# Kernel optimization log

Hardware: AMD Instinct MI355X
Metric: run time of the kernel (lower is better)

Reference implementation:

```python
import jax, jax.numpy as jnp
import numpy as np

N_NODES = 100000
N_EDGES = 1600000
D_FEAT = 128
HIDDEN = 64
N_CLASSES = 40
NEG_SLOPE = 0.01  # jax.nn.leaky_relu default, matches flax nn.leaky_relu


def glorot(key, shape):
    fan_in, fan_out = shape
    return jax.random.normal(key, shape, dtype=jnp.float32) * jnp.sqrt(2.0 / (fan_in + fan_out))


def setup_inputs() -> dict:
    key = jax.random.key(0)
    ks = jax.random.split(key, 8)
    nodes = jax.random.normal(ks[0], (N_NODES, D_FEAT), dtype=jnp.float32)
    senders = jax.random.randint(ks[1], (N_EDGES,), 0, N_NODES, dtype=jnp.int32)
    receivers = jax.random.randint(ks[2], (N_EDGES,), 0, N_NODES, dtype=jnp.int32)
    W1 = glorot(ks[3], (D_FEAT, HIDDEN))
    b1 = jnp.zeros((HIDDEN,), jnp.float32)
    W2 = glorot(ks[4], (HIDDEN, HIDDEN))
    b2 = jnp.zeros((HIDDEN,), jnp.float32)
    W3 = glorot(ks[5], (HIDDEN, N_CLASSES))
    b3 = jnp.zeros((N_CLASSES,), jnp.float32)
    return {"nodes": nodes, "senders": senders, "receivers": receivers,
            "W1": W1, "b1": b1, "W2": W2, "b2": b2, "W3": W3, "b3": b3}


def gcn_aggregate(x, senders, receivers, n_nodes):
    """jraph.GraphConvolution symmetric_normalization aggregation (post update_node_fn)."""
    ones = jnp.ones(senders.shape[0], dtype=x.dtype)
    sender_deg = jax.ops.segment_sum(ones, senders, num_segments=n_nodes)
    receiver_deg = jax.ops.segment_sum(ones, receivers, num_segments=n_nodes)
    x = x * jax.lax.rsqrt(jnp.maximum(sender_deg, 1.0))[:, None]
    x = jax.ops.segment_sum(x[senders], receivers, num_segments=n_nodes)  # [N, F]
    x = x * jax.lax.rsqrt(jnp.maximum(receiver_deg, 1.0))[:, None]
    return x


def reference(nodes, senders, receivers, W1, b1, W2, b2, W3, b3):
    n = nodes.shape[0]
    # Layer 1: GraphConvolution(MLP([hidden, hidden], leaky_relu))
    h = jax.nn.leaky_relu(nodes @ W1 + b1, NEG_SLOPE)
    h = jax.nn.leaky_relu(h @ W2 + b2, NEG_SLOPE)
    h = gcn_aggregate(h, senders, receivers, n)
    # Dropout is deterministic (training=False) -> identity
    # Layer 2: GraphConvolution(Dense(number_classes))
    h = h @ W3 + b3
    h = gcn_aggregate(h, senders, receivers, n)
    return jax.nn.softmax(h, axis=-1)
```

## Files before the change

### kernel.cpp

```cpp
#include <hip/hip_runtime.h>
#include <hip/hip_fp16.h>

#define NEG_SLOPE 0.01f
#define RANGE_BITS 15
#define RANGE (1 << RANGE_BITS)
#define HWORDS (RANGE / 2)
#define SLICE_BITS 16
#define SLICE (1 << SLICE_BITS)

typedef _Float16 f16x8 __attribute__((ext_vector_type(8)));
typedef float f32x4 __attribute__((ext_vector_type(4)));

__device__ __forceinline__ float lrelu(float x) { return x > 0.f ? x : NEG_SLOPE * x; }

__device__ __forceinline__ unsigned pack2h(float a, float b) {
    __half2 h = __floats2half2_rn(a, b);
    unsigned u; __builtin_memcpy(&u, &h, 4); return u;
}
__device__ __forceinline__ float2 unpack2(unsigned u) {
    __half2 h = *reinterpret_cast<__half2*>(&u);
    return __half22float2(h);
}
__device__ __forceinline__ f16x8 u4h8(uint4 u) {
    f16x8 r; __builtin_memcpy(&r, &u, 16); return r;
}

__global__ __launch_bounds__(1024) void count_kernel(
    const int* __restrict__ snd, const int* __restrict__ rcv,
    unsigned* __restrict__ partial, unsigned short* __restrict__ pos16,
    int nE, int NR, int NS)
{
    __shared__ unsigned hist[HWORDS];
    const int b = blockIdx.x;
    const int a = b / (NR * NS);
    const int rem = b - a * NR * NS;
    const int r = rem / NS;
    const int s = rem - r * NS;
    const int t = threadIdx.x;
    for (int k = t; k < HWORDS; k += 1024) hist[k] = 0u;
    __syncthreads();
    const int base = r << RANGE_BITS;
    const int lo = s << SLICE_BITS;
    const int hi = min(lo + SLICE, nE);
    if (a == 0) {
        for (int i = lo + t; i < hi; i += 1024) {
            const int v = rcv[i];
            const unsigned d = (unsigned)(v - base);
            if (d < (unsigned)RANGE) {
                const unsigned sh = (d & 1u) << 4;
                const unsigned old = atomicAdd(&hist[d >> 1], 1u << sh);
                pos16[i] = (unsigned short)((old >> sh) & 0xffffu);
            }
        }
    } else {
        for (int i = lo + t; i < hi; i += 1024) {
            const int v = snd[i];
            const unsigned d = (unsigned)(v - base);
            if (d < (unsigned)RANGE) atomicAdd(&hist[d >> 1], 1u << ((d & 1u) << 4));
        }
    }
    __syncthreads();
    unsigned* dst = partial + (size_t)((a * NR + r) * NS + s) * HWORDS;
    for (int k = t; k < HWORDS; k += 1024) dst[k] = hist[k];
}

__global__ __launch_bounds__(256) void scanp_kernel(
    unsigned* __restrict__ partial,
    int* __restrict__ dr_i,
    float* __restrict__ rin, float* __restrict__ rout,
    int nN, int NR, int NS)
{
    const int gid = blockIdx.x * 256 + threadIdx.x;
    if (gid >= NR * HWORDS) return;
    const int r  = gid >> (RANGE_BITS - 1);
    const int wd = gid & (HWORDS - 1);
    unsigned* prcv = partial + (size_t)(r * NS) * HWORDS + wd;
    unsigned run0 = 0, run1 = 0;
    for (int s = 0; s < NS; ++s) {
        unsigned* p = prcv + (size_t)s * HWORDS;
        const unsigned c = *p;
        *p = run0 | (run1 << 16);
        run0 += c & 0xffffu;
        run1 += c >> 16;
    }
    const unsigned* psnd = partial + (size_t)((NR + r) * NS) * HWORDS + wd;
    unsigned t0 = 0, t1 = 0;
    for (int s = 0; s < NS; ++s) {
        const unsigned c = psnd[(size_t)s * HWORDS];
        t0 += c & 0xffffu;
        t1 += c >> 16;
    }
    const int n0 = (r << RANGE_BITS) + 2 * wd;
    if (n0 < nN) {
        dr_i[n0] = (int)run0;
        rout[n0] = rsqrtf(fmaxf((float)run0, 1.f));
        rin[n0]  = rsqrtf(fmaxf((float)t0, 1.f));
    }
    if (n0 + 1 < nN) {
        dr_i[n0 + 1] = (int)run1;
        rout[n0 + 1] = rsqrtf(fmaxf((float)run1, 1.f));
        rin[n0 + 1]  = rsqrtf(fmaxf((float)t1, 1.f));
    }
}

__global__ __launch_bounds__(256) void scan1_kernel(const int* __restrict__ cnt,
                                                    int* __restrict__ rowptr,
                                                    int* __restrict__ bsums, int n)
{
    __shared__ int sd[256];
    const int t = threadIdx.x;
    const int base = blockIdx.x * 1024 + t * 4;
    int v0 = (base + 0 < n) ? cnt[base + 0] : 0;
    int v1 = (base + 1 < n) ? cnt[base + 1] : 0;
    int v2 = (base + 2 < n) ? cnt[base + 2] : 0;
    int v3 = (base + 3 < n) ? cnt[base + 3] : 0;
    const int p1 = v0, p2 = v0 + v1, p3 = v0 + v1 + v2;
    const int tot = p3 + v3;
    sd[t] = tot;
    __syncthreads();
    for (int off = 1; off < 256; off <<= 1) {
        int y = (t >= off) ? sd[t - off] : 0;
        __syncthreads();
        sd[t] += y;
        __syncthreads();
    }
    const int excl = sd[t] - tot;
    if (base + 0 < n) rowptr[base + 0] = excl;
    if (base + 1 < n) rowptr[base + 1] = excl + p1;
    if (base + 2 < n) rowptr[base + 2] = excl + p2;
    if (base + 3 < n) rowptr[base + 3] = excl + p3;
    if (t == 255) bsums[blockIdx.x] = sd[255];
}

__global__ __launch_bounds__(256) void scan2_kernel(int* __restrict__ bsums, int nb)
{
    __shared__ int sd[256];
    const int t = threadIdx.x;
    const int v = (t < nb) ? bsums[t] : 0;
    sd[t] = v;
    __syncthreads();
    for (int off = 1; off < 256; off <<= 1) {
        int y = (t >= off) ? sd[t - off] : 0;
        __syncthreads();
        sd[t] += y;
        __syncthreads();
    }
    if (t < nb) bsums[t] = sd[t] - v;
}

__global__ __launch_bounds__(256) void scan3_kernel(int* __restrict__ rowptr,
                                                    const int* __restrict__ bsums,
                                                    int n, int nE)
{
    const int gid = blockIdx.x * 256 + threadIdx.x;
    if (gid < n) rowptr[gid] += bsums[gid >> 10];
    if (gid == 0) rowptr[n] = nE;
}

__global__ __launch_bounds__(256) void fill_kernel(
    const int* __restrict__ snd, const int* __restrict__ rcv,
    const unsigned short* __restrict__ pos16, const unsigned* __restrict__ partial,
    const int* __restrict__ rowptr, int* __restrict__ csr_src,
    int nE, int NS)
{
    const int i = blockIdx.x * 256 + threadIdx.x;
    if (i >= nE) return;
    const int rv = rcv[i];
    const int r = rv >> RANGE_BITS;
    const int s = i >> SLICE_BITS;
    const unsigned pw = partial[(size_t)(r * NS + s) * HWORDS + ((rv & (RANGE - 1)) >> 1)];
    const int pref = (int)((pw >> ((rv & 1) << 4)) & 0xffffu);
    const int pos = rowptr[rv] + pref + (int)pos16[i];
    csr_src[pos] = snd[i];
}

__global__ __launch_bounds__(256) void mlp_kernel(
    const float* __restrict__ X, const float* __restrict__ W1, const float* __restrict__ b1,
    const float* __restrict__ W2, const float* __restrict__ b2, const float* __restrict__ W3,
    const float* __restrict__ rin, __half* __restrict__ p, int nN)
{
    __shared__ uint4 R1[1024];
    __shared__ uint4 R2[512];

    const int t    = threadIdx.x;
    const int w    = t >> 6;
    const int l    = t & 63;
    const int lrow = l & 15;
    const int lq   = l >> 4;
    const int row0 = blockIdx.x * 64;

    {
        const int c = l;
        for (int ch = 0; ch < 4; ++ch) {
            const int kc = 4 * w + ch;
            const float* wp = W1 + (kc * 8) * 64 + c;
            uint4 u;
            u.x = pack2h(wp[0],       wp[64]);
            u.y = pack2h(wp[2 * 64],  wp[3 * 64]);
            u.z = pack2h(wp[4 * 64],  wp[5 * 64]);
            u.w = pack2h(wp[6 * 64],  wp[7 * 64]);
            R1[c * 16 + (kc ^ (c & 7))] = u;
        }
    }
    __syncthreads();

    const int grow = row0 + 16 * w + lrow;
    const bool rowok = grow < nN;
    const float* xr = X + (size_t)grow * 128 + lq * 8;

    f32x4 acc1[4];
#pragma unroll
    for (int nt = 0; nt < 4; ++nt) acc1[nt] = (f32x4){0.f, 0.f, 0.f, 0.f};

#pragma unroll
    for (int ks = 0; ks < 4; ++ks) {
        float4 xa = make_float4(0.f, 0.f, 0.f, 0.f), xb = xa;
        if (rowok) {
            xa = *(const float4*)(xr + 32 * ks);
            xb = *(const float4*)(xr + 32 * ks + 4);
        }
        uint4 au;
        au.x = pack2h(xa.x, xa.y); au.y = pack2h(xa.z, xa.w);
        au.z = pack2h(xb.x, xb.y); au.w = pack2h(xb.z, xb.w);
        const f16x8 af = u4h8(au);
        const int kc = 4 * ks + lq;
#pragma unroll
        for (int nt = 0; nt < 4; ++nt) {
            const int c = 16 * nt + lrow;
            const uint4 bu = R1[c * 16 + (kc ^ (c & 7))];
            acc1[nt] = __builtin_amdgcn_mfma_f32_16x16x32_f16(af, u4h8(bu), acc1[nt], 0, 0, 0);
        }
    }
    __syncthreads();

    {
        __half* hh = (__half*)R2;
#pragma unroll
        for (int nt = 0; nt < 4; ++nt) {
            const int col = 16 * nt + lrow;
            const float bv = b1[col];
            const int ch = col >> 3, cl = col & 7;
#pragma unroll
            for (int r = 0; r < 4; ++r) {
                const int rw = 16 * w + 4 * lq + r;
                hh[rw * 64 + ((ch ^ (rw & 7)) * 8) + cl] = __float2half(lrelu(acc1[nt][r] + bv));
            }
        }
        const int c = l;
#pragma unroll
        for (int ch = 0; ch < 2; ++ch) {
            const int kc = 2 * w + ch;
            const float* wp = W2 + (kc * 8) * 64 + c;
            uint4 u;
            u.x = pack2h(wp[0],      wp[64]);
            u.y = pack2h(wp[2 * 64], wp[3 * 64]);
            u.z = pack2h(wp[4 * 64], wp[5 * 64]);
            u.w = pack2h(wp[6 * 64], wp[7 * 64]);
            R1[c * 8 + (kc ^ (c & 7))] = u;
        }
        if (c < 48) {
            const bool cv = c < 40;
#pragma unroll
            for (int ch = 0; ch < 2; ++ch) {
                const int kc = 2 * w + ch;
                const float* wp = W3 + (kc * 8) * 40 + c;
                uint4 u;
                u.x = pack2h(cv ? wp[0]      : 0.f, cv ? wp[40]     : 0.f);
                u.y = pack2h(cv ? wp[2 * 40] : 0.f, cv ? wp[3 * 40] : 0.f);
                u.z = pack2h(cv ? wp[4 * 40] : 0.f, cv ? wp[5 * 40] : 0.f);
                u.w = pack2h(cv ? wp[6 * 40] : 0.f, cv ? wp[7 * 40] : 0.f);
                R1[512 + c * 8 + (kc ^ (c & 7))] = u;
            }
        }
    }
    __syncthreads();

    f32x4 acc2[4];
#pragma unroll
    for (int nt = 0; nt < 4; ++nt) acc2[nt] = (f32x4){0.f, 0.f, 0.f, 0.f};
    {
        const int ar = 16 * w + lrow;
#pragma unroll
        for (int ks = 0; ks < 2; ++ks) {
            const int kc = 4 * ks + lq;
            const f16x8 af = u4h8(R2[ar * 8 + (kc ^ (ar & 7))]);
#pragma unroll
            for (int nt = 0; nt < 4; ++nt) {
                const int c = 16 * nt + lrow;
                const uint4 bu = R1[c * 8 + (kc ^ (c & 7))];
                acc2[nt] = __builtin_amdgcn_mfma_f32_16x16x32_f16(af, u4h8(bu), acc2[nt], 0, 0, 0);
            }
        }
    }
    __syncthreads();

    {
        __half* hh = (__half*)R2;
#pragma unroll
        for (int nt = 0; nt < 4; ++nt) {
            const int col = 16 * nt + lrow;
            const float bv = b2[col];
            const int ch = col >> 3, cl = col & 7;
#pragma unroll
            for (int r = 0; r < 4; ++r) {
                const int rw = 16 * w + 4 * lq + r;
                hh[rw * 64 + ((ch ^ (rw & 7)) * 8) + cl] = __float2half(lrelu(acc2[nt][r] + bv));
            }
        }
    }
    __syncthreads();

    f32x4 acc3[3];
#pragma unroll
    for (int nt = 0; nt < 3; ++nt) acc3[nt] = (f32x4){0.f, 0.f, 0.f, 0.f};
    {
        const int ar = 16 * w + lrow;
#pragma unroll
        for (int ks = 0; ks < 2; ++ks) {
            const int kc = 4 * ks + lq;
            const f16x8 af = u4h8(R2[ar * 8 + (kc ^ (ar & 7))]);
#pragma unroll
            for (int nt = 0; nt < 3; ++nt) {
                const int c = 16 * nt + lrow;
                const uint4 bu = R1[512 + c * 8 + (kc ^ (c & 7))];
                acc3[nt] = __builtin_amdgcn_mfma_f32_16x16x32_f16(af, u4h8(bu), acc3[nt], 0, 0, 0);
            }
        }
    }

#pragma unroll
    for (int r = 0; r < 4; ++r) {
        const int gr = row0 + 16 * w + 4 * lq + r;
        if (gr < nN) {
            const float rs = rin[gr];
            __half* pr = p + (size_t)gr * 40;
#pragma unroll
            for (int nt = 0; nt < 3; ++nt) {
                const int col = 16 * nt + lrow;
                if (col < 40) pr[col] = __float2half(acc3[nt][r] * rs);
            }
        }
    }
}

__global__ __launch_bounds__(256) void agg1_kernel(const __half* __restrict__ p,
                                                   const int* __restrict__ csr_src,
                                                   const int* __restrict__ rowptr,
                                                   const float* __restrict__ rin,
                                                   const float* __restrict__ rout,
                                                   __half* __restrict__ qbuf,
                                                   float* __restrict__ cbuf, int nN)
{
    const int gid = blockIdx.x * 256 + threadIdx.x;
    const int node = gid >> 3;
    const int j = gid & 7;
    if (node >= nN) return;
    const int beg = rowptr[node], end = rowptr[node + 1];
    const bool isch = (j < 5);
    const bool isr  = (j == 5);
    float a[8];
#pragma unroll
    for (int k = 0; k < 8; ++k) a[k] = 0.f;
    float cs = 0.f;

    for (int e = beg; e < end; e += 8) {
        int s[8];
#pragma unroll
        for (int b = 0; b < 8; ++b) {
            const int idx = e + b;
            s[b] = csr_src[idx < end ? idx : end - 1];
        }
        if (isch) {
            uint4 u[8];
#pragma unroll
            for (int b = 0; b < 8; ++b)
                u[b] = ((const uint4*)(p + (size_t)s[b] * 40))[j];
#pragma unroll
            for (int b = 0; b < 8; ++b) {
                if (e + b < end) {
                    float2 f;
                    f = unpack2(u[b].x); a[0] += f.x; a[1] += f.y;
                    f = unpack2(u[b].y); a[2] += f.x; a[3] += f.y;
                    f = unpack2(u[b].z); a[4] += f.x; a[5] += f.y;
                    f = unpack2(u[b].w); a[6] += f.x; a[7] += f.y;
                }
            }
        } else if (isr) {
            float rr[8];
#pragma unroll
            for (int b = 0; b < 8; ++b) rr[b] = rin[s[b]];
#pragma unroll
            for (int b = 0; b < 8; ++b)
                if (e + b < end) cs += rr[b];
        }
    }

    if (isch) {
        const float sc = rin[node] * rout[node];
        uint4 o;
        o.x = pack2h(a[0] * sc, a[1] * sc);
        o.y = pack2h(a[2] * sc, a[3] * sc);
        o.z = pack2h(a[4] * sc, a[5] * sc);
        o.w = pack2h(a[6] * sc, a[7] * sc);
        ((uint4*)(qbuf + (size_t)node * 40))[j] = o;
    } else if (isr) {
        cbuf[node] = cs * rout[node];
    }
}

__global__ __launch_bounds__(256) void agg2_kernel(const __half* __restrict__ qbuf,
                                                   const int* __restrict__ csr_src,
                                                   const int* __restrict__ rowptr,
                                                   const float* __restrict__ rout,
                                                   const float* __restrict__ cbuf,
                                                   const float* __restrict__ b3,
                                                   float* __restrict__ out, int nN)
{
    const int gid = blockIdx.x * 256 + threadIdx.x;
    const int node = gid >> 3;
    const int j = gid & 7;
    if (node >= nN) return;
    const int beg = rowptr[node], end = rowptr[node + 1];
    const bool isch = (j < 5);
    float a[8];
#pragma unroll
    for (int k = 0; k < 8; ++k) a[k] = 0.f;

    for (int e = beg; e < end; e += 8) {
        int s[8];
#pragma unroll
        for (int b = 0; b < 8; ++b) {
            const int idx = e + b;
            s[b] = csr_src[idx < end ? idx : end - 1];
        }
        if (isch) {
            uint4 u[8];
#pragma unroll
            for (int b = 0; b < 8; ++b)
                u[b] = ((const uint4*)(qbuf + (size_t)s[b] * 40))[j];
#pragma unroll
            for (int b = 0; b < 8; ++b) {
                if (e + b < end) {
                    float2 f;
                    f = unpack2(u[b].x); a[0] += f.x; a[1] += f.y;
                    f = unpack2(u[b].y); a[2] += f.x; a[3] += f.y;
                    f = unpack2(u[b].z); a[4] += f.x; a[5] += f.y;
                    f = unpack2(u[b].w); a[6] += f.x; a[7] += f.y;
                }
            }
        }
    }

    const float ro = rout[node];
    const float c  = cbuf[node];
    float z[8];
    float m = -1e30f, ssum = 0.f;
    if (isch) {
#pragma unroll
        for (int k = 0; k < 8; ++k) {
            z[k] = ro * a[k] + c * b3[j * 8 + k];
            m = fmaxf(m, z[k]);
        }
    }
    m = fmaxf(m, __shfl_xor(m, 1));
    m = fmaxf(m, __shfl_xor(m, 2));
    m = fmaxf(m, __shfl_xor(m, 4));
    if (isch) {
#pragma unroll
        for (int k = 0; k < 8; ++k) { z[k] = __expf(z[k] - m); ssum += z[k]; }
    }
    ssum += __shfl_xor(ssum, 1);
    ssum += __shfl_xor(ssum, 2);
    ssum += __shfl_xor(ssum, 4);
    if (isch) {
        const float inv = 1.f / ssum;
        float4* orow = (float4*)(out + (size_t)node * 40);
        orow[j * 2 + 0] = make_float4(z[0] * inv, z[1] * inv, z[2] * inv, z[3] * inv);
        orow[j * 2 + 1] = make_float4(z[4] * inv, z[5] * inv, z[6] * inv, z[7] * inv);
    }
}

extern "C" void kernel_launch(void* const* d_in, const int* in_sizes, int n_in,
                              void* d_out, int out_size, void* d_ws, size_t ws_size,
                              hipStream_t stream)
{
    const float* nodes = (const float*)d_in[0];
    const int*   snd   = (const int*)d_in[1];
    const int*   rcv   = (const int*)d_in[2];
    const float* W1    = (const float*)d_in[3];
    const float* b1    = (const float*)d_in[4];
    const float* W2    = (const float*)d_in[5];
    const float* b2    = (const float*)d_in[6];
    const float* W3    = (const float*)d_in[7];
    const float* b3    = (const float*)d_in[8];

    const int nN = in_sizes[0] / 128;
    const int nE = in_sizes[1];
    const int NR = (nN + RANGE - 1) >> RANGE_BITS;
    const int NS = (nE + SLICE - 1) >> SLICE_BITS;

    size_t off = 0;
    auto alloc = [&](size_t n) { size_t r = off; off += (n + 3) & ~(size_t)3; return r; };
    int*   dr_i    = (int*)d_ws + alloc(nN);
    int*   rowptr  = (int*)d_ws + alloc(nN + 1);
    int*   bsums   = (int*)d_ws + alloc(256);
    float* rin     = (float*)d_ws + alloc(nN);
    float* rout    = (float*)d_ws + alloc(nN);
    float* cbuf    = (float*)d_ws + alloc(nN);
    int*   csr_src = (int*)d_ws + alloc(nE);
    const size_t psz = (size_t)2 * NR * NS * HWORDS;
    size_t ubase = alloc(0);
    unsigned*       partial = (unsigned*)d_ws + ubase;
    unsigned short* pos16   = (unsigned short*)((unsigned*)d_ws + ubase + psz);
    __half* pbuf = (__half*)((int*)d_ws + ubase);
    __half* qbuf = pbuf + (size_t)nN * 40;

    const int nb1 = (nN + 1023) / 1024;

    count_kernel<<<2 * NR * NS, 1024, 0, stream>>>(snd, rcv, partial, pos16, nE, NR, NS);
    scanp_kernel<<<(NR * HWORDS + 255) / 256, 256, 0, stream>>>(partial, dr_i, rin, rout, nN, NR, NS);
    scan1_kernel<<<nb1, 256, 0, stream>>>(dr_i, rowptr, bsums, nN);
    scan2_kernel<<<1, 256, 0, stream>>>(bsums, nb1);
    scan3_kernel<<<(nN + 255) / 256, 256, 0, stream>>>(rowptr, bsums, nN, nE);
    fill_kernel<<<(nE + 255) / 256, 256, 0, stream>>>(snd, rcv, pos16, partial, rowptr, csr_src, nE, NS);
    mlp_kernel<<<(nN + 63) / 64, 256, 0, stream>>>(nodes, W1, b1, W2, b2, W3, rin, pbuf, nN);
    agg1_kernel<<<((size_t)nN * 8 + 255) / 256, 256, 0, stream>>>(pbuf, csr_src, rowptr, rin, rout, qbuf, cbuf, nN);
    agg2_kernel<<<((size_t)nN * 8 + 255) / 256, 256, 0, stream>>>(qbuf, csr_src, rowptr, rout, cbuf, b3, (float*)d_out, nN);
}
```

Before: 174.2 us.

## Split features into per-XCD column planes for aggregation and add separate softmax

Feature buffers are stored as five planes of 8 half-precision columns, laid out node-major within each plane. The aggregation blocks are remapped so that each XCD processes whole planes, which keeps each gathered plane (about 1.6MB) resident in that XCD's L2 instead of having every XCD touch the full 8MB table. Because one thread now owns a single plane, softmax no longer fits inside the aggregation kernel. It moves to a new kernel, which adds an extra fp32 intermediate buffer and one more launch. The count kernel also switches to vectorised int4 index loads.

```diff
diff --git a/kernel.cpp b/kernel.cpp
--- a/kernel.cpp
+++ b/kernel.cpp
@@ -42,10 +42,26 @@
     const int base = r << RANGE_BITS;
     const int lo = s << SLICE_BITS;
     const int hi = min(lo + SLICE, nE);
+    const int n4 = (hi - lo) >> 2;
+    const int* arr = (a == 0) ? rcv : snd;
+    const int4* arr4 = (const int4*)(arr + lo);
     if (a == 0) {
-        for (int i = lo + t; i < hi; i += 1024) {
-            const int v = rcv[i];
-            const unsigned d = (unsigned)(v - base);
+        for (int i4 = t; i4 < n4; i4 += 1024) {
+            const int4 v = arr4[i4];
+            const int ib = lo + i4 * 4;
+            int vv[4] = {v.x, v.y, v.z, v.w};
+#pragma unroll
+            for (int c = 0; c < 4; ++c) {
+                const unsigned d = (unsigned)(vv[c] - base);
+                if (d < (unsigned)RANGE) {
+                    const unsigned sh = (d & 1u) << 4;
+                    const unsigned old = atomicAdd(&hist[d >> 1], 1u << sh);
+                    pos16[ib + c] = (unsigned short)((old >> sh) & 0xffffu);
+                }
+            }
+        }
+        for (int i = lo + n4 * 4 + t; i < hi; i += 1024) {
+            const unsigned d = (unsigned)(arr[i] - base);
             if (d < (unsigned)RANGE) {
                 const unsigned sh = (d & 1u) << 4;
                 const unsigned old = atomicAdd(&hist[d >> 1], 1u << sh);
@@ -53,9 +69,17 @@
             }
         }
     } else {
-        for (int i = lo + t; i < hi; i += 1024) {
-            const int v = snd[i];
-            const unsigned d = (unsigned)(v - base);
+        for (int i4 = t; i4 < n4; i4 += 1024) {
+            const int4 v = arr4[i4];
+            int vv[4] = {v.x, v.y, v.z, v.w};
+#pragma unroll
+            for (int c = 0; c < 4; ++c) {
+                const unsigned d = (unsigned)(vv[c] - base);
+                if (d < (unsigned)RANGE) atomicAdd(&hist[d >> 1], 1u << ((d & 1u) << 4));
+            }
+        }
+        for (int i = lo + n4 * 4 + t; i < hi; i += 1024) {
+            const unsigned d = (unsigned)(arr[i] - base);
             if (d < (unsigned)RANGE) atomicAdd(&hist[d >> 1], 1u << ((d & 1u) << 4));
         }
     }
@@ -333,11 +357,11 @@
         const int gr = row0 + 16 * w + 4 * lq + r;
         if (gr < nN) {
             const float rs = rin[gr];
-            __half* pr = p + (size_t)gr * 40;
 #pragma unroll
             for (int nt = 0; nt < 3; ++nt) {
                 const int col = 16 * nt + lrow;
-                if (col < 40) pr[col] = __float2half(acc3[nt][r] * rs);
+                if (col < 40)
+                    p[((size_t)(col >> 3) * nN + gr) * 8 + (col & 7)] = __float2half(acc3[nt][r] * rs);
             }
         }
     }
@@ -349,15 +373,20 @@
                                                    const float* __restrict__ rin,
                                                    const float* __restrict__ rout,
                                                    __half* __restrict__ qbuf,
-                                                   float* __restrict__ cbuf, int nN)
-{
-    const int gid = blockIdx.x * 256 + threadIdx.x;
-    const int node = gid >> 3;
-    const int j = gid & 7;
+                                                   float* __restrict__ cbuf,
+                                                   int nN, int NB, int PER_XCD)
+{
+    const int b = blockIdx.x;
+    const int xcd = b & 7;
+    const int unit = xcd * PER_XCD + (b >> 3);
+    if (unit >= 5 * NB) return;
+    const int plane = unit / NB;
+    const int nb = unit - plane * NB;
+    const int node = nb * 256 + threadIdx.x;
     if (node >= nN) return;
     const int beg = rowptr[node], end = rowptr[node + 1];
-    const bool isch = (j < 5);
-    const bool isr  = (j == 5);
+    const uint4* pp = (const uint4*)p + (size_t)plane * nN;
+    const bool dorin = (plane == 0);
     float a[8];
 #pragma unroll
     for (int k = 0; k < 8; ++k) a[k] = 0.f;
@@ -366,46 +395,39 @@
     for (int e = beg; e < end; e += 8) {
         int s[8];
 #pragma unroll
-        for (int b = 0; b < 8; ++b) {
-            const int idx = e + b;
-            s[b] = csr_src[idx < end ? idx : end - 1];
-        }
-        if (isch) {
-            uint4 u[8];
-#pragma unroll
-            for (int b = 0; b < 8; ++b)
-                u[b] = ((const uint4*)(p + (size_t)s[b] * 40))[j];
-#pragma unroll
-            for (int b = 0; b < 8; ++b) {
-                if (e + b < end) {
-                    float2 f;
-                    f = unpack2(u[b].x); a[0] += f.x; a[1] += f.y;
-                    f = unpack2(u[b].y); a[2] += f.x; a[3] += f.y;
-                    f = unpack2(u[b].z); a[4] += f.x; a[5] += f.y;
-                    f = unpack2(u[b].w); a[6] += f.x; a[7] += f.y;
-                }
-            }
-        } else if (isr) {
-            float rr[8];
-#pragma unroll
-            for (int b = 0; b < 8; ++b) rr[b] = rin[s[b]];
-#pragma unroll
-            for (int b = 0; b < 8; ++b)
-                if (e + b < end) cs += rr[b];
-        }
-    }
-
-    if (isch) {
-        const float sc = rin[node] * rout[node];
-        uint4 o;
-        o.x = pack2h(a[0] * sc, a[1] * sc);
-        o.y = pack2h(a[2] * sc, a[3] * sc);
-        o.z = pack2h(a[4] * sc, a[5] * sc);
-        o.w = pack2h(a[6] * sc, a[7] * sc);
-        ((uint4*)(qbuf + (size_t)node * 40))[j] = o;
-    } else if (isr) {
-        cbuf[node] = cs * rout[node];
-    }
+        for (int bb = 0; bb < 8; ++bb) {
+            const int idx = e + bb;
+            s[bb] = csr_src[idx < end ? idx : end - 1];
+        }
+        uint4 u[8];
+#pragma unroll
+        for (int bb = 0; bb < 8; ++bb) u[bb] = pp[s[bb]];
+        float rr[8];
+        if (dorin) {
+#pragma unroll
+            for (int bb = 0; bb < 8; ++bb) rr[bb] = rin[s[bb]];
+        }
+#pragma unroll
+        for (int bb = 0; bb < 8; ++bb) {
+            if (e + bb < end) {
+                float2 f;
+                f = unpack2(u[bb].x); a[0] += f.x; a[1] += f.y;
+                f = unpack2(u[bb].y); a[2] += f.x; a[3] += f.y;
+                f = unpack2(u[bb].z); a[4] += f.x; a[5] += f.y;
+                f = unpack2(u[bb].w); a[6] += f.x; a[7] += f.y;
+                if (dorin) cs += rr[bb];
+            }
+        }
+    }
+
+    const float sc = rin[node] * rout[node];
+    uint4 o;
+    o.x = pack2h(a[0] * sc, a[1] * sc);
+    o.y = pack2h(a[2] * sc, a[3] * sc);
+    o.z = pack2h(a[4] * sc, a[5] * sc);
+    o.w = pack2h(a[6] * sc, a[7] * sc);
+    ((uint4*)qbuf)[(size_t)plane * nN + node] = o;
+    if (dorin) cbuf[node] = cs * rout[node];
 }
 
 __global__ __launch_bounds__(256) void agg2_kernel(const __half* __restrict__ qbuf,
@@ -414,14 +436,19 @@
                                                    const float* __restrict__ rout,
                                                    const float* __restrict__ cbuf,
                                                    const float* __restrict__ b3,
-                                                   float* __restrict__ out, int nN)
-{
-    const int gid = blockIdx.x * 256 + threadIdx.x;
-    const int node = gid >> 3;
-    const int j = gid & 7;
+                                                   float* __restrict__ zbuf,
+                                                   int nN, int NB, int PER_XCD)
+{
+    const int b = blockIdx.x;
+    const int xcd = b & 7;
+    const int unit = xcd * PER_XCD + (b >> 3);
+    if (unit >= 5 * NB) return;
+    const int plane = unit / NB;
+    const int nb = unit - plane * NB;
+    const int node = nb * 256 + threadIdx.x;
     if (node >= nN) return;
     const int beg = rowptr[node], end = rowptr[node + 1];
-    const bool isch = (j < 5);
+    const uint4* qp = (const uint4*)qbuf + (size_t)plane * nN;
     float a[8];
 #pragma unroll
     for (int k = 0; k < 8; ++k) a[k] = 0.f;
@@ -429,55 +456,66 @@
     for (int e = beg; e < end; e += 8) {
         int s[8];
 #pragma unroll
-        for (int b = 0; b < 8; ++b) {
-            const int idx = e + b;
-            s[b] = csr_src[idx < end ? idx : end - 1];
-        }
-        if (isch) {
-            uint4 u[8];
-#pragma unroll
-            for (int b = 0; b < 8; ++b)
-                u[b] = ((const uint4*)(qbuf + (size_t)s[b] * 40))[j];
-#pragma unroll
-            for (int b = 0; b < 8; ++b) {
-                if (e + b < end) {
-                    float2 f;
-                    f = unpack2(u[b].x); a[0] += f.x; a[1] += f.y;
-                    f = unpack2(u[b].y); a[2] += f.x; a[3] += f.y;
-                    f = unpack2(u[b].z); a[4] += f.x; a[5] += f.y;
-                    f = unpack2(u[b].w); a[6] += f.x; a[7] += f.y;
-                }
+        for (int bb = 0; bb < 8; ++bb) {
+            const int idx = e + bb;
+            s[bb] = csr_src[idx < end ? idx : end - 1];
+        }
+        uint4 u[8];
+#pragma unroll
+        for (int bb = 0; bb < 8; ++bb) u[bb] = qp[s[bb]];
+#pragma unroll
+        for (int bb = 0; bb < 8; ++bb) {
+            if (e + bb < end) {
+                float2 f;
+                f = unpack2(u[bb].x); a[0] += f.x; a[1] += f.y;
+                f = unpack2(u[bb].y); a[2] += f.x; a[3] += f.y;
+                f = unpack2(u[bb].z); a[4] += f.x; a[5] += f.y;
+                f = unpack2(u[bb].w); a[6] += f.x; a[7] += f.y;
             }
         }
     }
 
     const float ro = rout[node];
     const float c  = cbuf[node];
-    float z[8];
-    float m = -1e30f, ssum = 0.f;
-    if (isch) {
-#pragma unroll
-        for (int k = 0; k < 8; ++k) {
-            z[k] = ro * a[k] + c * b3[j * 8 + k];
-            m = fmaxf(m, z[k]);
-        }
-    }
-    m = fmaxf(m, __shfl_xor(m, 1));
-    m = fmaxf(m, __shfl_xor(m, 2));
-    m = fmaxf(m, __shfl_xor(m, 4));
-    if (isch) {
-#pragma unroll
-        for (int k = 0; k < 8; ++k) { z[k] = __expf(z[k] - m); ssum += z[k]; }
-    }
-    ssum += __shfl_xor(ssum, 1);
-    ssum += __shfl_xor(ssum, 2);
-    ssum += __shfl_xor(ssum, 4);
-    if (isch) {
-        const float inv = 1.f / ssum;
-        float4* orow = (float4*)(out + (size_t)node * 40);
-        orow[j * 2 + 0] = make_float4(z[0] * inv, z[1] * inv, z[2] * inv, z[3] * inv);
-        orow[j * 2 + 1] = make_float4(z[4] * inv, z[5] * inv, z[6] * inv, z[7] * inv);
-    }
+    float4 z0, z1;
+    z0.x = ro * a[0] + c * b3[plane * 8 + 0];
+    z0.y = ro * a[1] + c * b3[plane * 8 + 1];
+    z0.z = ro * a[2] + c * b3[plane * 8 + 2];
+    z0.w = ro * a[3] + c * b3[plane * 8 + 3];
+    z1.x = ro * a[4] + c * b3[plane * 8 + 4];
+    z1.y = ro * a[5] + c * b3[plane * 8 + 5];
+    z1.z = ro * a[6] + c * b3[plane * 8 + 6];
+    z1.w = ro * a[7] + c * b3[plane * 8 + 7];
+    float4* zp = (float4*)zbuf + ((size_t)plane * nN + node) * 2;
+    zp[0] = z0;
+    zp[1] = z1;
+}
+
+__global__ __launch_bounds__(256) void softmax_kernel(const float* __restrict__ zbuf,
+                                                      float* __restrict__ out, int nN)
+{
+    const int node = blockIdx.x * 256 + threadIdx.x;
+    if (node >= nN) return;
+    float v[40];
+#pragma unroll
+    for (int c = 0; c < 5; ++c) {
+        const float4* zp = (const float4*)zbuf + ((size_t)c * nN + node) * 2;
+        const float4 a = zp[0], b = zp[1];
+        v[c * 8 + 0] = a.x; v[c * 8 + 1] = a.y; v[c * 8 + 2] = a.z; v[c * 8 + 3] = a.w;
+        v[c * 8 + 4] = b.x; v[c * 8 + 5] = b.y; v[c * 8 + 6] = b.z; v[c * 8 + 7] = b.w;
+    }
+    float m = v[0];
+#pragma unroll
+    for (int c = 1; c < 40; ++c) m = fmaxf(m, v[c]);
+    float s = 0.f;
+#pragma unroll
+    for (int c = 0; c < 40; ++c) { v[c] = __expf(v[c] - m); s += v[c]; }
+    const float inv = 1.f / s;
+    float4* orow = (float4*)(out + (size_t)node * 40);
+#pragma unroll
+    for (int c4 = 0; c4 < 10; ++c4)
+        orow[c4] = make_float4(v[c4 * 4 + 0] * inv, v[c4 * 4 + 1] * inv,
+                               v[c4 * 4 + 2] * inv, v[c4 * 4 + 3] * inv);
 }
 
 extern "C" void kernel_launch(void* const* d_in, const int* in_sizes, int n_in,
@@ -498,6 +536,9 @@
     const int nE = in_sizes[1];
     const int NR = (nN + RANGE - 1) >> RANGE_BITS;
     const int NS = (nE + SLICE - 1) >> SLICE_BITS;
+    const int NB = (nN + 255) >> 8;
+    const int UNITS = 5 * NB;
+    const int PER_XCD = (UNITS + 7) / 8;
 
     size_t off = 0;
     auto alloc = [&](size_t n) { size_t r = off; off += (n + 3) & ~(size_t)3; return r; };
@@ -514,6 +555,7 @@
     unsigned short* pos16   = (unsigned short*)((unsigned*)d_ws + ubase + psz);
     __half* pbuf = (__half*)((int*)d_ws + ubase);
     __half* qbuf = pbuf + (size_t)nN * 40;
+    float*  zbuf = (float*)(qbuf + (size_t)nN * 40);
 
     const int nb1 = (nN + 1023) / 1024;
 
@@ -524,6 +566,7 @@
     scan3_kernel<<<(nN + 255) / 256, 256, 0, stream>>>(rowptr, bsums, nN, nE);
     fill_kernel<<<(nE + 255) / 256, 256, 0, stream>>>(snd, rcv, pos16, partial, rowptr, csr_src, nE, NS);
     mlp_kernel<<<(nN + 63) / 64, 256, 0, stream>>>(nodes, W1, b1, W2, b2, W3, rin, pbuf, nN);
-    agg1_kernel<<<((size_t)nN * 8 + 255) / 256, 256, 0, stream>>>(pbuf, csr_src, rowptr, rin, rout, qbuf, cbuf, nN);
-    agg2_kernel<<<((size_t)nN * 8 + 255) / 256, 256, 0, stream>>>(qbuf, csr_src, rowptr, rout, cbuf, b3, (float*)d_out, nN);
-}
+    agg1_kernel<<<8 * PER_XCD, 256, 0, stream>>>(pbuf, csr_src, rowptr, rin, rout, qbuf, cbuf, nN, NB, PER_XCD);
+    agg2_kernel<<<8 * PER_XCD, 256, 0, stream>>>(qbuf, csr_src, rowptr, rout, cbuf, b3, zbuf, nN, NB, PER_XCD);
+    softmax_kernel<<<(nN + 255) / 256, 256, 0, stream>>>(zbuf, (float*)d_out, nN);
+}
```

New measurement: 223.9 us. +28.5%, slower.
